# Kernel optimization log

Measured on AMD Instinct MI355X. Metric: run time of the kernel, lower is better.

The kernel has to match this reference:

```python
import jax, jax.numpy as jnp
import numpy as np

N = 50000      # nodes
E = 800000     # edges (avg degree 16)
IN_DIM = 64
EMB = 64
L = 4          # num_layer
BN_EPS = 1e-5


def setup_inputs() -> dict:
    key = jax.random.key(0)
    ks = jax.random.split(key, 8)
    s = 0.05
    return {
        "x": jax.random.normal(ks[0], (N, 1, IN_DIM), jnp.float32),
        "edge_index": jax.random.randint(ks[1], (2, E), 0, N, jnp.int32),
        "edge_attr": jax.random.normal(ks[2], (E, 3), jnp.float32),
        "edge_weight": jax.random.uniform(ks[3], (E,), jnp.float32),
        # atom encoder Linear(in_dim, emb)
        "ae_w": jax.random.normal(ks[4], (IN_DIM, EMB), jnp.float32) * s,
        "ae_b": jnp.zeros((EMB,), jnp.float32),
        # per-layer GIN MLP: Linear -> BN -> ReLU -> Linear (stacked over L)
        "W1": jax.random.normal(ks[5], (L, EMB, EMB), jnp.float32) * s,
        "b1": jnp.zeros((L, EMB), jnp.float32),
        "g1": jnp.ones((L, EMB), jnp.float32),
        "be1": jnp.zeros((L, EMB), jnp.float32),
        "W2": jax.random.normal(ks[6], (L, EMB, EMB), jnp.float32) * s,
        "b2": jnp.zeros((L, EMB), jnp.float32),
        # outer per-layer BatchNorm1d in GNN_node
        "g_out": jnp.ones((L, EMB), jnp.float32),
        "be_out": jnp.zeros((L, EMB), jnp.float32),
    }


def _bn(h, g, b):
    # BatchNorm1d, training mode: batch stats over node dim, biased variance
    m = h.mean(0)
    v = h.var(0)
    return (h - m) * jax.lax.rsqrt(v + BN_EPS) * g + b


def reference(x, edge_index, edge_attr, edge_weight,
              ae_w, ae_b, W1, b1, g1, be1, W2, b2, g_out, be_out):
    # atom encoder on x[:, 0] : [N, in_dim] -> [N, emb]
    h = x[:, 0] @ ae_w + ae_b
    src = edge_index[0]
    dst = edge_index[1]
    n = h.shape[0]
    num_layers = W1.shape[0]
    for l in range(num_layers):
        # MyPyGINConv (train_eps=False, eps=0): scatter-add of x_j * w_e, plus self term
        msg = h[src] * edge_weight[:, None]                      # [E, emb]
        agg = jax.ops.segment_sum(msg, dst, num_segments=n)      # [N, emb]
        out = agg + h                                            # (1+eps)*x_r, eps=0
        # conv MLP: Linear -> BN -> ReLU -> Linear
        out = jax.nn.relu(_bn(out @ W1[l] + b1[l], g1[l], be1[l]))
        out = out @ W2[l] + b2[l]
        # outer BN + ReLU (always applied for 'originalgin'); dropout p=0; residual
        out = jax.nn.relu(_bn(out, g_out[l], be_out[l]))
        h = out + h
    return h  # JK='last'
```

## Files before the change

### kernel.cpp

```cpp
#include <hip/hip_runtime.h>
#include <stdint.h>

#define EMB 64
#define BN_EPS 1e-5f
#define BSH 8
#define CHUNK 4096
#define TS 68

typedef short bfrag __attribute__((ext_vector_type(8)));
typedef float f32x4 __attribute__((ext_vector_type(4)));

#define IN_F32    0
#define IN_BF16   1
#define IN_BF16BN 2

struct SMM {
  float tb[64 * TS];
  float st[128];
  float scs[EMB], shs[EMB];
  unsigned short wb[4096];
};

__device__ __forceinline__ unsigned short f2b(float x) {
  unsigned u = __float_as_uint(x);
  u += 0x7FFFu + ((u >> 16) & 1u);
  return (unsigned short)(u >> 16);
}
__device__ __forceinline__ float b2f(unsigned short v) {
  return __uint_as_float(((unsigned)v) << 16);
}

__device__ __forceinline__ void enc_tile(SMM& sm, int tile,
    const float* x, const float* aewf, const float* bias,
    unsigned short* out16, int N) {
  const int tid = threadIdx.x;
  const int lane = tid & 63;
  const int wv = tid >> 6;
  const int r = wv >> 1;
  const int c0 = (wv & 1) * 2;
  const int m = lane & 15;
  const int quad = lane >> 4;
  const int node0 = tile * 64;

#pragma unroll
  for (int it = 0; it < 8; it++) {
    int idx = it * 512 + tid;
    int j = idx >> 6, k = idx & 63;
    sm.wb[idx] = f2b(aewf[k * EMB + j]);
  }
  __syncthreads();

  bfrag a0 = {0, 0, 0, 0, 0, 0, 0, 0}, a1 = {0, 0, 0, 0, 0, 0, 0, 0};
  const int arow = node0 + r * 16 + m;
  if (arow < N) {
    const float4* af4 = (const float4*)(x + (size_t)arow * EMB + quad * 8);
    float4 f0 = af4[0], f1 = af4[1];
    float4 f2 = af4[8], f3 = af4[9];
    a0[0] = (short)f2b(f0.x); a0[1] = (short)f2b(f0.y);
    a0[2] = (short)f2b(f0.z); a0[3] = (short)f2b(f0.w);
    a0[4] = (short)f2b(f1.x); a0[5] = (short)f2b(f1.y);
    a0[6] = (short)f2b(f1.z); a0[7] = (short)f2b(f1.w);
    a1[0] = (short)f2b(f2.x); a1[1] = (short)f2b(f2.y);
    a1[2] = (short)f2b(f2.z); a1[3] = (short)f2b(f2.w);
    a1[4] = (short)f2b(f3.x); a1[5] = (short)f2b(f3.y);
    a1[6] = (short)f2b(f3.z); a1[7] = (short)f2b(f3.w);
  }
  f32x4 zz[2];
#pragma unroll
  for (int cc = 0; cc < 2; cc++) {
    const int c = c0 + cc;
    const unsigned short* bb = &sm.wb[(c * 16 + m) * EMB + quad * 8];
    bfrag b0 = *(const bfrag*)bb;
    bfrag b1 = *(const bfrag*)(bb + 32);
    f32x4 z = {0.f, 0.f, 0.f, 0.f};
    z = __builtin_amdgcn_mfma_f32_16x16x32_bf16(a0, b0, z, 0, 0, 0);
    z = __builtin_amdgcn_mfma_f32_16x16x32_bf16(a1, b1, z, 0, 0, 0);
    zz[cc] = z;
  }
#pragma unroll
  for (int cc = 0; cc < 2; cc++) {
    const int c = c0 + cc;
    float bj = bias[c * 16 + m];
#pragma unroll
    for (int reg = 0; reg < 4; reg++) {
      int row = r * 16 + quad * 4 + reg;
      float v = (node0 + row < N) ? (zz[cc][reg] + bj) : 0.f;
      sm.tb[row * TS + c * 16 + m] = v;
    }
  }
  __syncthreads();
  ushort4* o4 = (ushort4*)(out16 + (size_t)node0 * EMB);
#pragma unroll
  for (int it = 0; it < 2; it++) {
    int flat4 = it * 512 + tid;
    int nsub = flat4 >> 4;
    int c4 = flat4 & 15;
    if (node0 + nsub < N) {
      const float* s4 = sm.tb + nsub * TS + c4 * 4;
      ushort4 o;
      o.x = f2b(s4[0]); o.y = f2b(s4[1]);
      o.z = f2b(s4[2]); o.w = f2b(s4[3]);
      o4[flat4] = o;
    }
  }
}

__global__ void __launch_bounds__(512) k_enc_prep(
        const float* __restrict__ x, const float* __restrict__ ae_w,
        const float* __restrict__ ae_b,
        const float* __restrict__ W1, const float* __restrict__ W2,
        unsigned short* __restrict__ Wt16, int* __restrict__ hist_part,
        float* __restrict__ stats, const int* __restrict__ ei,
        unsigned short* __restrict__ hb16,
        int E, int L, int nstats, int ntiles, int nchunks, int N) {
  __shared__ SMM sm;
  if ((int)blockIdx.x < ntiles) {
    enc_tile(sm, blockIdx.x, x, ae_w, ae_b, hb16, N);
    return;
  }
  const int pb = blockIdx.x - ntiles;
  const int tid = threadIdx.x;
  int* lh = (int*)sm.tb;
  const int nw2 = 2 * L * EMB * EMB;
  for (int gid = pb * 512 + tid; gid < nw2; gid += nchunks * 512) {
    int mI = gid >> 12;
    int j = (gid >> 6) & 63;
    int k = gid & 63;
    const float* src = (mI < L) ? W1 + (size_t)mI * EMB * EMB
                                : W2 + (size_t)(mI - L) * EMB * EMB;
    Wt16[EMB * EMB + gid] = f2b(src[k * EMB + j]);
  }
  for (int i = pb * 512 + tid; i < nstats; i += nchunks * 512) stats[i] = 0.0f;
  if (tid < 256) lh[tid] = 0;
  __syncthreads();
  const int c0 = pb * CHUNK;
  const int cend = min(c0 + CHUNK, E);
  for (int e = c0 + tid; e < cend; e += 512)
    atomicAdd(&lh[((unsigned)ei[E + e]) >> BSH], 1);
  __syncthreads();
  if (tid < 256) hist_part[pb * 256 + tid] = lh[tid];
}

__global__ void __launch_bounds__(256) k_part(
        const int* __restrict__ ei, const float* __restrict__ ew,
        const int* __restrict__ hist_part, int* __restrict__ bbase,
        int2* __restrict__ eG, int E, int nchunks, int nb) {
  __shared__ int a[256], lbase[256], loff[256];
  const int t = threadIdx.x;
  const int c = blockIdx.x;
  int pre = 0, post = 0;
#pragma unroll 8
  for (int cc = 0; cc < c; cc++) pre += hist_part[cc * 256 + t];
#pragma unroll 8
  for (int cc = c; cc < nchunks; cc++) post += hist_part[cc * 256 + t];
  const int tot = pre + post;
  a[t] = tot;
  __syncthreads();
  for (int off = 1; off < 256; off <<= 1) {
    int x = (t >= off) ? a[t - off] : 0;
    __syncthreads();
    a[t] += x;
    __syncthreads();
  }
  int excl = a[t] - tot;
  lbase[t] = excl + pre;
  loff[t] = 0;
  if (c == 0 && t <= nb) bbase[t] = excl;
  __syncthreads();
  const int c0 = c * CHUNK;
#pragma unroll 4
  for (int i = 0; i < 16; i++) {
    int e = c0 + i * 256 + t;
    if (e < E) {
      int d = ei[E + e];
      int g = ((unsigned)d) >> BSH;
      int pk = ei[e] | ((d & 255) << 24);
      int pos = lbase[g] + atomicAdd(&loff[g], 1);
      eG[pos] = make_int2(pk, __float_as_int(ew[e]));
    }
  }
}

__global__ void __launch_bounds__(256) k_build(
        const int2* __restrict__ eG, const int* __restrict__ bbase,
        int* __restrict__ rowst, int* __restrict__ counts,
        int2* __restrict__ pairs, int N) {
  __shared__ int lcnt[256], a[256], lcur[256];
  const int t = threadIdx.x;
  const int b = blockIdx.x;
  const int e0 = bbase[b], e1 = bbase[b + 1];
  lcnt[t] = 0;
  __syncthreads();
  for (int i = e0 + t; i < e1; i += 256)
    atomicAdd(&lcnt[((unsigned)eG[i].x) >> 24], 1);
  __syncthreads();
  int v = lcnt[t];
  a[t] = v;
  __syncthreads();
  for (int off = 1; off < 256; off <<= 1) {
    int x = (t >= off) ? a[t - off] : 0;
    __syncthreads();
    a[t] += x;
    __syncthreads();
  }
  int excl = a[t] - v;
  lcur[t] = excl;
  int node = (b << BSH) + t;
  if (node < N) { rowst[node] = e0 + excl; counts[node] = v; }
  __syncthreads();
  for (int i = e0 + t; i < e1; i += 256) {
    int2 p = eG[i];
    int loc = ((unsigned)p.x) >> 24;
    int pos = e0 + atomicAdd(&lcur[loc], 1);
    pairs[pos] = make_int2(p.x & 0x00FFFFFF, p.y);
  }
}

__global__ void k_agg(const unsigned short* __restrict__ hb,
                      const int* __restrict__ rowst,
                      const int* __restrict__ counts, const int2* __restrict__ pairs,
                      unsigned short* __restrict__ out16, int N) {
  const int lane = threadIdx.x & 63;
  const int half = lane >> 5;
  const int col = lane & 31;
  int wave = (blockIdx.x * blockDim.x + threadIdx.x) >> 6;
  const int nwaves = (gridDim.x * blockDim.x) >> 6;
  for (int nA = wave; nA < N; nA += 2 * nwaves) {
    const int nB = nA + nwaves;
    const int uA = __builtin_amdgcn_readfirstlane(nA);
    const int uB = __builtin_amdgcn_readfirstlane(nB);
    const bool hasB = uB < N;
    int sA = rowst[uA], eA = sA + counts[uA];
    int sB = 0, eB = 0;
    if (hasB) { sB = rowst[uB]; eB = sB + counts[uB]; }
    float a0A[4] = {0, 0, 0, 0}, a1A[4] = {0, 0, 0, 0};
    float a0B[4] = {0, 0, 0, 0}, a1B[4] = {0, 0, 0, 0};
    for (int xA = sA, xB = sB; (xA < eA) | (xB < eB); xA += 8, xB += 8) {
      int2 pA[8], pB[8];
#pragma unroll
      for (int k = 0; k < 8; k++) {
        int ia = xA + k;
        pA[k] = pairs[ia < eA ? ia : 0];
      }
#pragma unroll
      for (int k = 0; k < 8; k++) {
        int ib = xB + k;
        pB[k] = pairs[ib < eB ? ib : 0];
      }
#pragma unroll
      for (int j = 0; j < 4; j++) {
        int2 pp = half ? pA[2 * j + 1] : pA[2 * j];
        bool ok = (xA + 2 * j + half) < eA;
        float w = ok ? __int_as_float(pp.y) : 0.f;
        unsigned v = *((const unsigned*)(hb + (size_t)pp.x * EMB) + col);
        a0A[j] = fmaf(w, b2f((unsigned short)(v & 0xFFFFu)), a0A[j]);
        a1A[j] = fmaf(w, b2f((unsigned short)(v >> 16)), a1A[j]);
      }
#pragma unroll
      for (int j = 0; j < 4; j++) {
        int2 pp = half ? pB[2 * j + 1] : pB[2 * j];
        bool ok = (xB + 2 * j + half) < eB;
        float w = ok ? __int_as_float(pp.y) : 0.f;
        unsigned v = *((const unsigned*)(hb + (size_t)pp.x * EMB) + col);
        a0B[j] = fmaf(w, b2f((unsigned short)(v & 0xFFFFu)), a0B[j]);
        a1B[j] = fmaf(w, b2f((unsigned short)(v >> 16)), a1B[j]);
      }
    }
    {
      float s0 = (a0A[0] + a0A[1]) + (a0A[2] + a0A[3]);
      float s1 = (a1A[0] + a1A[1]) + (a1A[2] + a1A[3]);
      s0 += __shfl_xor(s0, 32);
      s1 += __shfl_xor(s1, 32);
      float v0 = __shfl(s0, lane >> 1);
      float v1 = __shfl(s1, lane >> 1);
      float sum = ((lane & 1) ? v1 : v0) + b2f(hb[(size_t)uA * EMB + lane]);
      out16[(size_t)uA * EMB + lane] = f2b(sum);
    }
    if (hasB) {
      float s0 = (a0B[0] + a0B[1]) + (a0B[2] + a0B[3]);
      float s1 = (a1B[0] + a1B[1]) + (a1B[2] + a1B[3]);
      s0 += __shfl_xor(s0, 32);
      s1 += __shfl_xor(s1, 32);
      float v0 = __shfl(s0, lane >> 1);
      float v1 = __shfl(s1, lane >> 1);
      float sum = ((lane & 1) ? v1 : v0) + b2f(hb[(size_t)uB * EMB + lane]);
      out16[(size_t)uB * EMB + lane] = f2b(sum);
    }
  }
}

__global__ void k_aggbn(const unsigned short* __restrict__ u16,
                        const unsigned short* __restrict__ hold,
                        const float* __restrict__ st,
                        const float* __restrict__ g, const float* __restrict__ be,
                        const int* __restrict__ rowst,
                        const int* __restrict__ counts,
                        const int2* __restrict__ pairs,
                        unsigned short* __restrict__ hnew,
                        unsigned short* __restrict__ out16,
                        float invN, int N) {
  __shared__ float scs[EMB], shs[EMB];
  const int tid = threadIdx.x;
  if (tid < EMB) {
    float s1 = 0.f, s2 = 0.f;
#pragma unroll
    for (int k = 0; k < 8; k++) {
      s1 += st[k * 128 + tid];
      s2 += st[k * 128 + 64 + tid];
    }
    float mu = s1 * invN;
    float va = fmaf(s2, invN, -mu * mu);
    float rs = rsqrtf(va + BN_EPS);
    float sc = rs * g[tid];
    scs[tid] = sc;
    shs[tid] = fmaf(-mu, sc, be[tid]);
  }
  __syncthreads();
  const int lane = tid & 63;
  const int half = lane >> 5;
  const int col = lane & 31;
  const float sc0 = scs[2 * col], sc1 = scs[2 * col + 1];
  const float sh0 = shs[2 * col], sh1 = shs[2 * col + 1];
  const float scl = scs[lane], shl = shs[lane];
  int wave = (blockIdx.x * blockDim.x + tid) >> 6;
  const int nwaves = (gridDim.x * blockDim.x) >> 6;
  for (int nA = wave; nA < N; nA += 2 * nwaves) {
    const int nB = nA + nwaves;
    const int uA = __builtin_amdgcn_readfirstlane(nA);
    const int uB = __builtin_amdgcn_readfirstlane(nB);
    const bool hasB = uB < N;
    int sA = rowst[uA], eA = sA + counts[uA];
    int sB = 0, eB = 0;
    if (hasB) { sB = rowst[uB]; eB = sB + counts[uB]; }
    float hnA = fmaxf(0.f, fmaf(b2f(u16[(size_t)uA * EMB + lane]), scl, shl)) +
                b2f(hold[(size_t)uA * EMB + lane]);
    float hnB = 0.f;
    if (hasB)
      hnB = fmaxf(0.f, fmaf(b2f(u16[(size_t)uB * EMB + lane]), scl, shl)) +
            b2f(hold[(size_t)uB * EMB + lane]);
    float a0A[4] = {0, 0, 0, 0}, a1A[4] = {0, 0, 0, 0};
    float a0B[4] = {0, 0, 0, 0}, a1B[4] = {0, 0, 0, 0};
    for (int xA = sA, xB = sB; (xA < eA) | (xB < eB); xA += 8, xB += 8) {
      int2 pA[8], pB[8];
#pragma unroll
      for (int k = 0; k < 8; k++) {
        int ia = xA + k;
        pA[k] = pairs[ia < eA ? ia : 0];
      }
#pragma unroll
      for (int k = 0; k < 8; k++) {
        int ib = xB + k;
        pB[k] = pairs[ib < eB ? ib : 0];
      }
#pragma unroll
      for (int j = 0; j < 4; j++) {
        int2 p = half ? pA[2 * j + 1] : pA[2 * j];
        bool ok = (xA + 2 * j + half) < eA;
        float w = ok ? __int_as_float(p.y) : 0.f;
        const size_t base = (size_t)p.x * EMB;
        unsigned vu = *((const unsigned*)(u16 + base) + col);
        unsigned vh = *((const unsigned*)(hold + base) + col);
        float h0 = fmaxf(0.f, fmaf(b2f((unsigned short)(vu & 0xFFFFu)), sc0, sh0))
                   + b2f((unsigned short)(vh & 0xFFFFu));
        float h1 = fmaxf(0.f, fmaf(b2f((unsigned short)(vu >> 16)), sc1, sh1))
                   + b2f((unsigned short)(vh >> 16));
        a0A[j] = fmaf(w, h0, a0A[j]);
        a1A[j] = fmaf(w, h1, a1A[j]);
      }
#pragma unroll
      for (int j = 0; j < 4; j++) {
        int2 p = half ? pB[2 * j + 1] : pB[2 * j];
        bool ok = (xB + 2 * j + half) < eB;
        float w = ok ? __int_as_float(p.y) : 0.f;
        const size_t base = (size_t)p.x * EMB;
        unsigned vu = *((const unsigned*)(u16 + base) + col);
        unsigned vh = *((const unsigned*)(hold + base) + col);
        float h0 = fmaxf(0.f, fmaf(b2f((unsigned short)(vu & 0xFFFFu)), sc0, sh0))
                   + b2f((unsigned short)(vh & 0xFFFFu));
        float h1 = fmaxf(0.f, fmaf(b2f((unsigned short)(vu >> 16)), sc1, sh1))
                   + b2f((unsigned short)(vh >> 16));
        a0B[j] = fmaf(w, h0, a0B[j]);
        a1B[j] = fmaf(w, h1, a1B[j]);
      }
    }
    {
      float s0 = (a0A[0] + a0A[1]) + (a0A[2] + a0A[3]);
      float s1 = (a1A[0] + a1A[1]) + (a1A[2] + a1A[3]);
      s0 += __shfl_xor(s0, 32);
      s1 += __shfl_xor(s1, 32);
      float v0 = __shfl(s0, lane >> 1);
      float v1 = __shfl(s1, lane >> 1);
      float sum = ((lane & 1) ? v1 : v0) + hnA;
      out16[(size_t)uA * EMB + lane] = f2b(sum);
      hnew[(size_t)uA * EMB + lane] = f2b(hnA);
    }
    if (hasB) {
      float s0 = (a0B[0] + a0B[1]) + (a0B[2] + a0B[3]);
      float s1 = (a1B[0] + a1B[1]) + (a1B[2] + a1B[3]);
      s0 += __shfl_xor(s0, 32);
      s1 += __shfl_xor(s1, 32);
      float v0 = __shfl(s0, lane >> 1);
      float v1 = __shfl(s1, lane >> 1);
      float sum = ((lane & 1) ? v1 : v0) + hnB;
      out16[(size_t)uB * EMB + lane] = f2b(sum);
      hnew[(size_t)uB * EMB + lane] = f2b(hnB);
    }
  }
}

template <int INMODE, bool DO_STATS>
__global__ void __launch_bounds__(256) k_mmx(
        const void* __restrict__ in_v, const unsigned short* __restrict__ Wt,
        const float* __restrict__ bias, const float* __restrict__ stats,
        const float* __restrict__ g, const float* __restrict__ be, float invN,
        unsigned short* __restrict__ out16, float* __restrict__ st_out, int N) {
  __shared__ float tb[64 * TS];
  __shared__ float st_part[128];
  __shared__ float scs[EMB], shs[EMB];
  const int tid = threadIdx.x;
  const int lane = tid & 63;
  const int wv = tid >> 6;
  const int node0 = blockIdx.x * 64;
  const int m = lane & 15;
  const int quad = lane >> 4;

  if (DO_STATS && tid < 128) st_part[tid] = 0.f;
  if (INMODE == IN_BF16BN) {
    if (tid < EMB) {
      float s1 = 0.f, s2 = 0.f;
#pragma unroll
      for (int k = 0; k < 8; k++) {
        s1 += stats[k * 128 + tid];
        s2 += stats[k * 128 + 64 + tid];
      }
      float mm = s1 * invN;
      float va = fmaf(s2, invN, -mm * mm);
      float rs = rsqrtf(va + BN_EPS);
      float sc = rs * g[tid];
      scs[tid] = sc;
      shs[tid] = fmaf(-mm, sc, be[tid]);
    }
    __syncthreads();
  }

  const int arow = node0 + wv * 16 + m;
  bfrag a0 = {0, 0, 0, 0, 0, 0, 0, 0}, a1 = {0, 0, 0, 0, 0, 0, 0, 0};
  if (arow < N) {
    if (INMODE == IN_BF16) {
      const unsigned short* ab =
          (const unsigned short*)in_v + (size_t)arow * EMB + quad * 8;
      a0 = *(const bfrag*)ab;
      a1 = *(const bfrag*)(ab + 32);
    } else if (INMODE == IN_BF16BN) {
      const unsigned short* ab =
          (const unsigned short*)in_v + (size_t)arow * EMB + quad * 8;
      bfrag r0 = *(const bfrag*)ab;
      bfrag r1 = *(const bfrag*)(ab + 32);
#pragma unroll
      for (int j = 0; j < 8; j++) {
        int k0 = quad * 8 + j;
        float v0 = b2f((unsigned short)r0[j]);
        float v1 = b2f((unsigned short)r1[j]);
        v0 = fmaxf(0.f, fmaf(v0, scs[k0], shs[k0]));
        v1 = fmaxf(0.f, fmaf(v1, scs[k0 + 32], shs[k0 + 32]));
        a0[j] = (short)f2b(v0);
        a1[j] = (short)f2b(v1);
      }
    }
  }

  const unsigned short* bb = Wt + (size_t)m * EMB + quad * 8;
  f32x4 acc[4];
#pragma unroll
  for (int c = 0; c < 4; c++) {
    bfrag b0 = *(const bfrag*)(bb + c * 16 * EMB);
    bfrag b1 = *(const bfrag*)(bb + c * 16 * EMB + 32);
    f32x4 z = {0.f, 0.f, 0.f, 0.f};
    z = __builtin_amdgcn_mfma_f32_16x16x32_bf16(a0, b0, z, 0, 0, 0);
    z = __builtin_amdgcn_mfma_f32_16x16x32_bf16(a1, b1, z, 0, 0, 0);
    acc[c] = z;
  }

#pragma unroll
  for (int c = 0; c < 4; c++) {
    float bj = bias[c * 16 + m];
#pragma unroll
    for (int r = 0; r < 4; r++) {
      int row = wv * 16 + quad * 4 + r;
      float v = (node0 + row < N) ? (acc[c][r] + bj) : 0.f;
      tb[row * TS + c * 16 + m] = v;
    }
  }
  __syncthreads();

  if (DO_STATS) {
    float ssum = 0.f, ssq = 0.f;
#pragma unroll
    for (int i = 0; i < 16; i++) {
      float v = tb[(wv * 16 + i) * TS + lane];
      ssum += v;
      ssq = fmaf(v, v, ssq);
    }
    atomicAdd(&st_part[lane], ssum);
    atomicAdd(&st_part[64 + lane], ssq);
  }

  ushort4* o4 = (ushort4*)(out16 + (size_t)node0 * EMB);
#pragma unroll
  for (int it = 0; it < 4; it++) {
    int flat4 = it * 256 + tid;
    int nsub = flat4 >> 4;
    int c4 = flat4 & 15;
    if (node0 + nsub < N) {
      const float* s4 = tb + nsub * TS + c4 * 4;
      ushort4 o;
      o.x = f2b(s4[0]); o.y = f2b(s4[1]);
      o.z = f2b(s4[2]); o.w = f2b(s4[3]);
      o4[flat4] = o;
    }
  }

  if (DO_STATS) {
    __syncthreads();
    if (tid < 128)
      atomicAdd(&st_out[((unsigned)blockIdx.x & 7u) * 128 + tid], st_part[tid]);
  }
}

__global__ void k_bnres_last(const unsigned short* __restrict__ u16,
                             const float* __restrict__ st,
                             const float* __restrict__ g,
                             const float* __restrict__ be,
                             const unsigned short* __restrict__ hb16,
                             float* __restrict__ out32,
                             float invN, int total4) {
  __shared__ float scs[EMB], shs[EMB];
  const int tid = threadIdx.x;
  if (tid < EMB) {
    float s1 = 0.f, s2 = 0.f;
#pragma unroll
    for (int k = 0; k < 8; k++) {
      s1 += st[k * 128 + tid];
      s2 += st[k * 128 + 64 + tid];
    }
    float mm = s1 * invN;
    float va = fmaf(s2, invN, -mm * mm);
    float rs = rsqrtf(va + BN_EPS);
    float sc = rs * g[tid];
    scs[tid] = sc;
    shs[tid] = fmaf(-mm, sc, be[tid]);
  }
  __syncthreads();
  int stride = gridDim.x * blockDim.x;
  for (int i4 = blockIdx.x * blockDim.x + tid; i4 < total4; i4 += stride) {
    int c4 = i4 & 15;
    ushort4 uv = ((const ushort4*)u16)[i4];
    ushort4 hv = ((const ushort4*)hb16)[i4];
    float4 scv = *(const float4*)&scs[c4 * 4];
    float4 shv = *(const float4*)&shs[c4 * 4];
    float4 o;
    o.x = fmaxf(0.f, fmaf(b2f(uv.x), scv.x, shv.x)) + b2f(hv.x);
    o.y = fmaxf(0.f, fmaf(b2f(uv.y), scv.y, shv.y)) + b2f(hv.y);
    o.z = fmaxf(0.f, fmaf(b2f(uv.z), scv.z, shv.z)) + b2f(hv.z);
    o.w = fmaxf(0.f, fmaf(b2f(uv.w), scv.w, shv.w)) + b2f(hv.w);
    ((float4*)out32)[i4] = o;
  }
}

extern "C" void kernel_launch(void* const* d_in, const int* in_sizes, int n_in,
                              void* d_out, int out_size, void* d_ws, size_t ws_size,
                              hipStream_t stream) {
  const float* x     = (const float*)d_in[0];
  const int*   ei    = (const int*)d_in[1];
  const float* ew    = (const float*)d_in[3];
  const float* ae_w  = (const float*)d_in[4];
  const float* ae_b  = (const float*)d_in[5];
  const float* W1    = (const float*)d_in[6];
  const float* b1    = (const float*)d_in[7];
  const float* g1    = (const float*)d_in[8];
  const float* be1   = (const float*)d_in[9];
  const float* W2    = (const float*)d_in[10];
  const float* b2    = (const float*)d_in[11];
  const float* g_out = (const float*)d_in[12];
  const float* be_out= (const float*)d_in[13];

  const int N = in_sizes[0] / EMB;
  const int E = in_sizes[3];
  const int L = in_sizes[6] / (EMB * EMB);
  const float invN = 1.0f / (float)N;
  const int NBUCK = (N + 255) >> BSH;
  const int nchunks = (E + CHUNK - 1) / CHUNK;

  uintptr_t p = (uintptr_t)d_ws;
  auto alloc = [&](size_t bytes) -> void* {
    p = (p + 255) & ~(uintptr_t)255;
    void* r = (void*)p;
    p += bytes;
    return r;
  };
  unsigned short* hbA  = (unsigned short*)alloc((size_t)N * EMB * 2);
  unsigned short* hbB  = (unsigned short*)alloc((size_t)N * EMB * 2);
  unsigned short* a16  = (unsigned short*)alloc((size_t)N * EMB * 2);
  unsigned short* t16  = (unsigned short*)alloc((size_t)N * EMB * 2);
  unsigned short* u16  = (unsigned short*)alloc((size_t)N * EMB * 2);
  unsigned short* Wt16 = (unsigned short*)alloc((size_t)(1 + 2 * L) * EMB * EMB * 2);
  int*   counts= (int*)alloc((size_t)N * 4);
  int*   rowst = (int*)alloc((size_t)N * 4);
  int*   hist_part = (int*)alloc((size_t)nchunks * 256 * 4);
  int*   bbase = (int*)alloc(257 * 4);
  int2*  pairs = (int2*)alloc((size_t)E * 8);
  int2*  eG    = (int2*)alloc((size_t)E * 8);
  float* stats = (float*)alloc((size_t)L * 2 * 8 * 128 * 4);
  (void)ws_size; (void)n_in; (void)out_size;

  const int ntiles = (N + 63) / 64;
  const int nstats = L * 2 * 8 * 128;

  hipLaunchKernelGGL(k_enc_prep, dim3(ntiles + nchunks), dim3(512), 0, stream,
                     x, ae_w, ae_b, W1, W2, Wt16, hist_part, stats, ei,
                     hbA, E, L, nstats, ntiles, nchunks, N);
  hipLaunchKernelGGL(k_part, dim3(nchunks), dim3(256), 0, stream,
                     ei, ew, hist_part, bbase, eG, E, nchunks, NBUCK);
  hipLaunchKernelGGL(k_build, dim3(NBUCK), dim3(256), 0, stream,
                     eG, bbase, rowst, counts, pairs, N);

  unsigned short* hcur = hbA;
  unsigned short* hnxt = hbB;
  for (int l = 0; l < L; l++) {
    float* stats1 = stats + (size_t)(l * 2 + 0) * 1024;
    float* stats2 = stats + (size_t)(l * 2 + 1) * 1024;

    if (l == 0) {
      hipLaunchKernelGGL(k_agg, dim3(2048), dim3(256), 0, stream,
                         hcur, rowst, counts, pairs, a16, N);
    } else {
      float* stats2p = stats + (size_t)((l - 1) * 2 + 1) * 1024;
      hipLaunchKernelGGL(k_aggbn, dim3(2048), dim3(256), 0, stream,
                         u16, hcur, stats2p, g_out + (size_t)(l - 1) * EMB,
                         be_out + (size_t)(l - 1) * EMB, rowst, counts, pairs,
                         hnxt, a16, invN, N);
      unsigned short* tmp = hcur; hcur = hnxt; hnxt = tmp;
    }
    hipLaunchKernelGGL((k_mmx<IN_BF16, true>), dim3(ntiles), dim3(256), 0, stream,
                       a16, Wt16 + (size_t)(1 + l) * EMB * EMB, b1 + (size_t)l * EMB,
                       (const float*)nullptr, (const float*)nullptr,
                       (const float*)nullptr, 0.f, t16, stats1, N);
    hipLaunchKernelGGL((k_mmx<IN_BF16BN, true>), dim3(ntiles), dim3(256), 0, stream,
                       t16, Wt16 + (size_t)(1 + L + l) * EMB * EMB, b2 + (size_t)l * EMB,
                       stats1, g1 + (size_t)l * EMB, be1 + (size_t)l * EMB, invN,
                       u16, stats2, N);
  }
  hipLaunchKernelGGL(k_bnres_last, dim3(1024), dim3(256), 0, stream,
                     u16, stats + (size_t)((L - 1) * 2 + 1) * 1024,
                     g_out + (size_t)(L - 1) * EMB, be_out + (size_t)(L - 1) * EMB,
                     hcur, (float*)d_out, invN, N * 16);
}
```

Baseline: 366.0 us.

## Build CSR with global per-node atomics instead of two-level bucket partition

The two-pass bucketed partition (chunk histogram, then partition into eG, then per-bucket local sort) is replaced by three simpler steps. First, per-node degree counts are taken with global atomics. A scan kernel then computes row starts, with each block recomputing the bucket prefix itself. Finally, a scatter kernel places edges directly into their CSR slots using global atomic cursors. This drops the intermediate eG buffer and one full read/write pass over the edges, at the cost of heavier global atomic traffic and redundant bucket-sum reads in every scan block.

```diff
diff --git a/kernel.cpp b/kernel.cpp
--- a/kernel.cpp
+++ b/kernel.cpp
@@ -3,7 +3,6 @@
 
 #define EMB 64
 #define BN_EPS 1e-5f
-#define BSH 8
 #define CHUNK 4096
 #define TS 68
 
@@ -109,7 +108,7 @@
         const float* __restrict__ x, const float* __restrict__ ae_w,
         const float* __restrict__ ae_b,
         const float* __restrict__ W1, const float* __restrict__ W2,
-        unsigned short* __restrict__ Wt16, int* __restrict__ hist_part,
+        unsigned short* __restrict__ Wt16, int* __restrict__ counts,
         float* __restrict__ stats, const int* __restrict__ ei,
         unsigned short* __restrict__ hb16,
         int E, int L, int nstats, int ntiles, int nchunks, int N) {
@@ -120,7 +119,6 @@
   }
   const int pb = blockIdx.x - ntiles;
   const int tid = threadIdx.x;
-  int* lh = (int*)sm.tb;
   const int nw2 = 2 * L * EMB * EMB;
   for (int gid = pb * 512 + tid; gid < nw2; gid += nchunks * 512) {
     int mI = gid >> 12;
@@ -131,29 +129,22 @@
     Wt16[EMB * EMB + gid] = f2b(src[k * EMB + j]);
   }
   for (int i = pb * 512 + tid; i < nstats; i += nchunks * 512) stats[i] = 0.0f;
-  if (tid < 256) lh[tid] = 0;
-  __syncthreads();
   const int c0 = pb * CHUNK;
   const int cend = min(c0 + CHUNK, E);
   for (int e = c0 + tid; e < cend; e += 512)
-    atomicAdd(&lh[((unsigned)ei[E + e]) >> BSH], 1);
-  __syncthreads();
-  if (tid < 256) hist_part[pb * 256 + tid] = lh[tid];
-}
-
-__global__ void __launch_bounds__(256) k_part(
-        const int* __restrict__ ei, const float* __restrict__ ew,
-        const int* __restrict__ hist_part, int* __restrict__ bbase,
-        int2* __restrict__ eG, int E, int nchunks, int nb) {
-  __shared__ int a[256], lbase[256], loff[256];
+    atomicAdd(&counts[ei[E + e]], 1);
+}
+
+__global__ void __launch_bounds__(256) k_scan(
+        const int* __restrict__ counts, int* __restrict__ rowst,
+        int* __restrict__ cur) {
+  __shared__ int a[256];
   const int t = threadIdx.x;
-  const int c = blockIdx.x;
-  int pre = 0, post = 0;
+  const int b = blockIdx.x;
+  int tot = 0;
+  const int* cb = counts + t * 256;
 #pragma unroll 8
-  for (int cc = 0; cc < c; cc++) pre += hist_part[cc * 256 + t];
-#pragma unroll 8
-  for (int cc = c; cc < nchunks; cc++) post += hist_part[cc * 256 + t];
-  const int tot = pre + post;
+  for (int i = 0; i < 256; i++) tot += cb[i];
   a[t] = tot;
   __syncthreads();
   for (int off = 1; off < 256; off <<= 1) {
@@ -162,57 +153,36 @@
     a[t] += x;
     __syncthreads();
   }
-  int excl = a[t] - tot;
-  lbase[t] = excl + pre;
-  loff[t] = 0;
-  if (c == 0 && t <= nb) bbase[t] = excl;
-  __syncthreads();
-  const int c0 = c * CHUNK;
+  const int bucketBase = (b == 0) ? 0 : a[b - 1];
+  __syncthreads();
+  int c = counts[b * 256 + t];
+  a[t] = c;
+  __syncthreads();
+  for (int off = 1; off < 256; off <<= 1) {
+    int x = (t >= off) ? a[t - off] : 0;
+    __syncthreads();
+    a[t] += x;
+    __syncthreads();
+  }
+  int excl = a[t] - c;
+  rowst[b * 256 + t] = bucketBase + excl;
+  cur[b * 256 + t] = 0;
+}
+
+__global__ void __launch_bounds__(256) k_scatter(
+        const int* __restrict__ ei, const float* __restrict__ ew,
+        const int* __restrict__ rowst, int* __restrict__ cur,
+        int2* __restrict__ pairs, int E) {
+  const int t = threadIdx.x;
+  const int c0 = blockIdx.x * CHUNK;
 #pragma unroll 4
   for (int i = 0; i < 16; i++) {
     int e = c0 + i * 256 + t;
     if (e < E) {
       int d = ei[E + e];
-      int g = ((unsigned)d) >> BSH;
-      int pk = ei[e] | ((d & 255) << 24);
-      int pos = lbase[g] + atomicAdd(&loff[g], 1);
-      eG[pos] = make_int2(pk, __float_as_int(ew[e]));
-    }
-  }
-}
-
-__global__ void __launch_bounds__(256) k_build(
-        const int2* __restrict__ eG, const int* __restrict__ bbase,
-        int* __restrict__ rowst, int* __restrict__ counts,
-        int2* __restrict__ pairs, int N) {
-  __shared__ int lcnt[256], a[256], lcur[256];
-  const int t = threadIdx.x;
-  const int b = blockIdx.x;
-  const int e0 = bbase[b], e1 = bbase[b + 1];
-  lcnt[t] = 0;
-  __syncthreads();
-  for (int i = e0 + t; i < e1; i += 256)
-    atomicAdd(&lcnt[((unsigned)eG[i].x) >> 24], 1);
-  __syncthreads();
-  int v = lcnt[t];
-  a[t] = v;
-  __syncthreads();
-  for (int off = 1; off < 256; off <<= 1) {
-    int x = (t >= off) ? a[t - off] : 0;
-    __syncthreads();
-    a[t] += x;
-    __syncthreads();
-  }
-  int excl = a[t] - v;
-  lcur[t] = excl;
-  int node = (b << BSH) + t;
-  if (node < N) { rowst[node] = e0 + excl; counts[node] = v; }
-  __syncthreads();
-  for (int i = e0 + t; i < e1; i += 256) {
-    int2 p = eG[i];
-    int loc = ((unsigned)p.x) >> 24;
-    int pos = e0 + atomicAdd(&lcur[loc], 1);
-    pairs[pos] = make_int2(p.x & 0x00FFFFFF, p.y);
+      int pos = rowst[d] + atomicAdd(&cur[d], 1);
+      pairs[pos] = make_int2(ei[e], __float_as_int(ew[e]));
+    }
   }
 }
 
@@ -588,7 +558,7 @@
   const int E = in_sizes[3];
   const int L = in_sizes[6] / (EMB * EMB);
   const float invN = 1.0f / (float)N;
-  const int NBUCK = (N + 255) >> BSH;
+  const int NBUCK = (N + 255) >> 8;
   const int nchunks = (E + CHUNK - 1) / CHUNK;
 
   uintptr_t p = (uintptr_t)d_ws;
@@ -604,25 +574,24 @@
   unsigned short* t16  = (unsigned short*)alloc((size_t)N * EMB * 2);
   unsigned short* u16  = (unsigned short*)alloc((size_t)N * EMB * 2);
   unsigned short* Wt16 = (unsigned short*)alloc((size_t)(1 + 2 * L) * EMB * EMB * 2);
-  int*   counts= (int*)alloc((size_t)N * 4);
-  int*   rowst = (int*)alloc((size_t)N * 4);
-  int*   hist_part = (int*)alloc((size_t)nchunks * 256 * 4);
-  int*   bbase = (int*)alloc(257 * 4);
+  int*   counts= (int*)alloc((size_t)256 * 256 * 4);
+  int*   rowst = (int*)alloc((size_t)NBUCK * 256 * 4);
+  int*   cur   = (int*)alloc((size_t)NBUCK * 256 * 4);
   int2*  pairs = (int2*)alloc((size_t)E * 8);
-  int2*  eG    = (int2*)alloc((size_t)E * 8);
   float* stats = (float*)alloc((size_t)L * 2 * 8 * 128 * 4);
   (void)ws_size; (void)n_in; (void)out_size;
 
   const int ntiles = (N + 63) / 64;
   const int nstats = L * 2 * 8 * 128;
 
+  hipMemsetAsync(counts, 0, (size_t)256 * 256 * 4, stream);
   hipLaunchKernelGGL(k_enc_prep, dim3(ntiles + nchunks), dim3(512), 0, stream,
-                     x, ae_w, ae_b, W1, W2, Wt16, hist_part, stats, ei,
+                     x, ae_w, ae_b, W1, W2, Wt16, counts, stats, ei,
                      hbA, E, L, nstats, ntiles, nchunks, N);
-  hipLaunchKernelGGL(k_part, dim3(nchunks), dim3(256), 0, stream,
-                     ei, ew, hist_part, bbase, eG, E, nchunks, NBUCK);
-  hipLaunchKernelGGL(k_build, dim3(NBUCK), dim3(256), 0, stream,
-                     eG, bbase, rowst, counts, pairs, N);
+  hipLaunchKernelGGL(k_scan, dim3(NBUCK), dim3(256), 0, stream,
+                     counts, rowst, cur);
+  hipLaunchKernelGGL(k_scatter, dim3(nchunks), dim3(256), 0, stream,
+                     ei, ew, rowst, cur, pairs, E);
 
   unsigned short* hcur = hbA;
   unsigned short* hnxt = hbB;
```

After: 423.8 us. +15.8%, slower.
